# Optimization experiments

Measured on AMD Instinct MI355X. Metric: run time of the kernel, lower is better.

Reference implementation:

```python
import jax, jax.numpy as jnp
import numpy as np
from jax import lax

B, N, FEAT, MID, HID, OUT = 128, 36, 2048, 517, 128, 1024
STEPS, TEMP = 3, 1.0


def setup_inputs() -> dict:
    key = jax.random.key(0)
    ks = jax.random.split(key, 10)
    s = 0.02
    return {
        "boxes": jax.random.uniform(ks[0], (B, 4, N), jnp.float32),
        "attention": jax.random.normal(ks[1], (B, N), jnp.float32),
        "features": jax.random.normal(ks[2], (B, N, FEAT), jnp.float32),
        "conv_w": jax.random.normal(ks[3], (MID - 5, FEAT), jnp.float32) * s,
        "conv_b": jnp.zeros((MID - 5,), jnp.float32),
        "skew_wx": jax.random.normal(ks[4], (HID, MID), jnp.float32) * s,
        "skew_wy": jax.random.normal(ks[5], (HID, MID), jnp.float32) * s,
        "skew_b1": jnp.zeros((HID,), jnp.float32),
        "skew_w2": jax.random.normal(ks[6], (HID,), jnp.float32) * s,
        "skew_b2": jnp.zeros((1,), jnp.float32),
        "w_ih": jax.random.normal(ks[7], (4 * OUT, MID), jnp.float32) * s,
        "w_hh": jax.random.normal(ks[8], (4 * OUT, OUT), jnp.float32) * s,
        "b_ih": jnp.zeros((4 * OUT,), jnp.float32),
        "b_hh": jnp.zeros((4 * OUT,), jnp.float32),
        "lr": jnp.ones((1,), jnp.float32),
    }


def _calculate_assignment(C, lr_abs, temp, steps):
    # C: (b, n, n) skew-symmetric ordering costs.
    logits = jnp.zeros_like(C)
    for _ in range(steps):
        P = jax.nn.softmax(logits / temp, axis=-1)  # position i -> distribution over elements l
        cum = jnp.cumsum(P, axis=1)                 # sum over positions k <= i
        below = cum - P                             # sum_{k<i} P_kl
        above = cum[:, -1:, :] - cum                # sum_{k>i} P_kl
        # grad_{ij} = sum_l C_{jl} * (above - below)_{il}  (uses skew-symmetry of C)
        G = jnp.einsum('bil,bjl->bij', above - below, C)
        logits = logits - lr_abs * G
    return jax.nn.softmax(logits / temp, axis=-1)


def reference(boxes, attention, features, conv_w, conv_b, skew_wx, skew_wy,
              skew_b1, skew_w2, skew_b2, w_ih, w_hh, b_ih, b_hh, lr):
    b = boxes.shape[0]
    # normalize boxes by per-sample max
    boxes = boxes / jnp.max(boxes.reshape(b, -1), axis=1)[:, None, None]
    # pointwise Conv1: 2048 -> MID-5, features arrives as (b, n, 2048)
    f = jnp.einsum('bnf,mf->bmn', features, conv_w) + conv_b[None, :, None]
    att = attention[:, None, :]                      # (b, 1, n)
    feats = jnp.concatenate([boxes, att, f], axis=1)  # (b, MID, n)
    # PairwiseSkew: f(x_i, x_j) - f(x_j, x_i); the first 1x1-conv over concatenated
    # pairs splits into two linear maps so we never materialize (b, 2*MID, n, n).
    hx = jnp.einsum('hm,bmn->bhn', skew_wx, feats)
    hy = jnp.einsum('hm,bmn->bhn', skew_wy, feats)
    h = jax.nn.relu(hx[:, :, :, None] + hy[:, :, None, :] + skew_b1[None, :, None, None])
    out = jnp.einsum('h,bhij->bij', skew_w2, h) + skew_b2[0]  # (b, n, n)
    C = out - jnp.swapaxes(out, 1, 2)  # skew-symmetrize
    A = _calculate_assignment(C, jnp.abs(lr)[0], TEMP, STEPS)
    # gate features by sigmoid(attention) and apply soft permutation
    gated = feats * jax.nn.sigmoid(att)               # (b, MID, n)
    x = jnp.einsum('bcl,bil->bci', gated, A)          # (b, MID, n)
    x_seq = jnp.transpose(x, (2, 0, 1))               # (n, b, MID)
    # single-layer LSTM (PyTorch gate order i, f, g, o); return final cell state
    bias = b_ih + b_hh
    Hd = w_hh.shape[1]
    def step(carry, xt):
        h_, c_ = carry
        gates = xt @ w_ih.T + h_ @ w_hh.T + bias
        i, fg, g, o = jnp.split(gates, 4, axis=-1)
        c_ = jax.nn.sigmoid(fg) * c_ + jax.nn.sigmoid(i) * jnp.tanh(g)
        h_ = jax.nn.sigmoid(o) * jnp.tanh(c_)
        return (h_, c_), None
    init = (jnp.zeros((b, Hd), x.dtype), jnp.zeros((b, Hd), x.dtype))
    (_, c_fin), _ = lax.scan(step, init, x_seq)
    return c_fin
```

## Files before the change

kernel.cpp:

```cpp
#include <hip/hip_runtime.h>
#include <math.h>

#define NB 128
#define NN 36
#define S37 37
#define S40 40
#define NFEAT 2048
#define NMID 517
#define KP 544
#define NHID 128
#define NOUT 1024
#define ROWS (NB*NN)

typedef __bf16 bf16x8 __attribute__((ext_vector_type(8)));
typedef float  f32x4  __attribute__((ext_vector_type(4)));

__device__ __forceinline__ float sigf(float x){ return 1.f/(1.f+expf(-x)); }
__device__ __forceinline__ unsigned short f2bf(float x){
    unsigned u = __float_as_uint(x);
    return (unsigned short)((u + 0x7FFFu + ((u>>16)&1u)) >> 16);
}
__device__ __forceinline__ float bf2f(unsigned short b){
    return __uint_as_float(((unsigned)b) << 16);
}

__global__ __launch_bounds__(256) void prep_all(
    const float* __restrict__ boxes, const float* __restrict__ att,
    const float* __restrict__ features, const float* __restrict__ conv_w,
    const float* __restrict__ wx, const float* __restrict__ wy,
    const float* __restrict__ b1, const float* __restrict__ w_ih,
    const float* __restrict__ w_hh, const float* __restrict__ b_ih,
    const float* __restrict__ b_hh,
    unsigned short* __restrict__ features_bf, unsigned short* __restrict__ convw_bf,
    unsigned short* __restrict__ wxy_bf, float* __restrict__ hxy_b,
    unsigned short* __restrict__ wih_il, unsigned short* __restrict__ whh_il,
    float* __restrict__ comb_b, unsigned short* __restrict__ h0,
    float* __restrict__ c, float* __restrict__ feats)
{
    int gtid = blockIdx.x*256 + threadIdx.x;
    int gs = gridDim.x*256;
    if (gtid < 128*64) {
        int b = gtid >> 6, t = gtid & 63;
        float mx = -1e30f;
        for (int idx = t; idx < 4*NN; idx += 64) mx = fmaxf(mx, boxes[b*4*NN + idx]);
        for (int off = 32; off > 0; off >>= 1) mx = fmaxf(mx, __shfl_down(mx, off));
        mx = __shfl(mx, 0);
        float inv = 1.f / mx;
        for (int idx = t; idx < 4*NN; idx += 64) {
            int r = idx / NN, n = idx - r*NN;
            feats[(size_t)(b*NN+n)*NMID + r] = boxes[b*4*NN + idx] * inv;
        }
        if (t < NN) feats[(size_t)(b*NN+t)*NMID + 4] = att[b*NN + t];
    }
    for (int i = gtid; i < ROWS*NFEAT; i += gs) features_bf[i] = f2bf(features[i]);
    for (int i = gtid; i < 512*NFEAT; i += gs) convw_bf[i] = f2bf(conv_w[i]);
    for (int i = gtid; i < 256*KP; i += gs) {
        int r = i / KP, k = i - r*KP;
        float v = 0.f;
        if (k < NMID) v = (r < NHID) ? wx[(size_t)r*NMID+k] : wy[(size_t)(r-NHID)*NMID+k];
        wxy_bf[i] = f2bf(v);
    }
    for (int i = gtid; i < 256; i += gs) hxy_b[i] = (i < NHID) ? b1[i] : 0.f;
    for (int i = gtid; i < 4*NOUT*KP; i += gs) {
        int row = i / KP, k = i - row*KP;
        int u = row >> 2, g = row & 3;
        wih_il[i] = (k < NMID) ? f2bf(w_ih[(size_t)(g*NOUT+u)*NMID + k]) : (unsigned short)0;
    }
    for (int i = gtid; i < 4*NOUT*NOUT; i += gs) {
        int row = i >> 10, k = i & 1023;
        int u = row >> 2, g = row & 3;
        whh_il[i] = f2bf(w_hh[(size_t)(g*NOUT+u)*NOUT + k]);
    }
    for (int i = gtid; i < 4*NOUT; i += gs) {
        int u = i >> 2, g = i & 3;
        comb_b[i] = b_ih[g*NOUT+u] + b_hh[g*NOUT+u];
    }
    for (int i = gtid; i < NB*NOUT; i += gs) { h0[i] = 0; c[i] = 0.f; }
}

__global__ __launch_bounds__(256) void gemm128(
    const unsigned short* __restrict__ A, const unsigned short* __restrict__ B,
    const float* __restrict__ bias, void* __restrict__ Cp,
    int Ksl, int lda, int ldb, int ldc, int obf, long long pstride)
{
    __shared__ __align__(16) char As[16384];
    __shared__ __align__(16) char Bs[16384];
    int m0 = blockIdx.y * 128, n0 = blockIdx.x * 128;
    int kbeg = blockIdx.z * Ksl;
    int tid = threadIdx.x;
    int lane = tid & 63, wave = tid >> 6;
    int wm = wave >> 1, wn = wave & 1;
    int sw = ((lane>>4)<<8) + (((lane&15) ^ ((lane>>4)<<2))<<4);
    f32x4 acc[4][4];
    #pragma unroll
    for (int i = 0; i < 4; ++i)
        #pragma unroll
        for (int j = 0; j < 4; ++j) acc[i][j] = (f32x4){0.f,0.f,0.f,0.f};

    for (int k0 = 0; k0 < Ksl; k0 += 32) {
        #pragma unroll
        for (int p = 0; p < 2; ++p) {
            int cc = p*256 + tid;
            int r = cc >> 2, q = cc & 3;
            int sa = ((r>>4)<<10) + (q<<8) + ((((r&15) ^ (q<<2)))<<4);
            uint4 va = *(const uint4*)(A + (size_t)(m0+r)*lda + kbeg + k0 + q*8);
            *(uint4*)(As + sa) = va;
            uint4 vb = *(const uint4*)(B + (size_t)(n0+r)*ldb + kbeg + k0 + q*8);
            *(uint4*)(Bs + sa) = vb;
        }
        __syncthreads();
        bf16x8 af[4], bfr[4];
        #pragma unroll
        for (int i = 0; i < 4; ++i) af[i]  = *(bf16x8*)(As + ((wm*4+i)<<10) + sw);
        #pragma unroll
        for (int j = 0; j < 4; ++j) bfr[j] = *(bf16x8*)(Bs + ((wn*4+j)<<10) + sw);
        #pragma unroll
        for (int i = 0; i < 4; ++i)
            #pragma unroll
            for (int j = 0; j < 4; ++j)
                acc[i][j] = __builtin_amdgcn_mfma_f32_16x16x32_bf16(af[i], bfr[j], acc[i][j], 0, 0, 0);
        __syncthreads();
    }
    int colf = lane & 15, rowq = lane >> 4;
    #pragma unroll
    for (int j = 0; j < 4; ++j) {
        int col = n0 + (wn*4+j)*16 + colf;
        float bv = bias ? bias[col] : 0.f;
        #pragma unroll
        for (int i = 0; i < 4; ++i) {
            #pragma unroll
            for (int reg = 0; reg < 4; ++reg) {
                int row = m0 + (wm*4+i)*16 + rowq*4 + reg;
                float v = acc[i][j][reg] + bv;
                if (obf) ((unsigned short*)Cp)[(size_t)row*ldc + col] = f2bf(v);
                else ((float*)Cp + (size_t)blockIdx.z*pstride)[(size_t)row*ldc + col] = v;
            }
        }
    }
}

__global__ __launch_bounds__(256) void conv_reduce(
    const float* __restrict__ part, const float* __restrict__ bias,
    float* __restrict__ feats, unsigned short* __restrict__ feats_bf)
{
    int gtid = blockIdx.x*256 + threadIdx.x;
    int gs = gridDim.x*256;
    const size_t PS = (size_t)ROWS * 512;
    for (int i = gtid; i < ROWS*512; i += gs) {
        int r = i >> 9, cc = i & 511;
        float s = part[i] + part[PS+i] + part[2*PS+i] + part[3*PS+i] + bias[cc];
        feats[(size_t)r*NMID + 5 + cc] = s;
        feats_bf[(size_t)r*KP + 5 + cc] = f2bf(s);
    }
    for (int i = gtid; i < ROWS*5; i += gs) {
        int r = i / 5, cc = i - r*5;
        feats_bf[(size_t)r*KP + cc] = f2bf(feats[(size_t)r*NMID + cc]);
    }
    for (int i = gtid; i < ROWS*27; i += gs) {
        int r = i / 27, cc = i - r*27;
        feats_bf[(size_t)r*KP + 517 + cc] = 0;
    }
}

__global__ __launch_bounds__(256) void gemm_mfma(
    const unsigned short* __restrict__ A, const unsigned short* __restrict__ B,
    const float* __restrict__ bias, void* __restrict__ Cp,
    int K, int lda, int ldb, int ldc, int obf)
{
    __shared__ __align__(16) char As[8192];
    __shared__ __align__(16) char Bs[4096];
    int m0 = blockIdx.y * 128, n0 = blockIdx.x * 64;
    int tid = threadIdx.x;
    int lane = tid & 63, wave = tid >> 6;
    int wm = wave >> 1, wn = wave & 1;
    f32x4 acc[4][2];
    #pragma unroll
    for (int i = 0; i < 4; ++i)
        #pragma unroll
        for (int j = 0; j < 2; ++j) acc[i][j] = (f32x4){0.f,0.f,0.f,0.f};

    for (int k0 = 0; k0 < K; k0 += 32) {
        #pragma unroll
        for (int cc = tid; cc < 512; cc += 256) {
            int r = cc >> 2, q = cc & 3;
            uint4 v = *(const uint4*)(A + (size_t)(m0+r)*lda + k0 + q*8);
            *(uint4*)(As + ((r>>4)<<10) + (q<<8) + ((r&15)<<4)) = v;
        }
        {
            int r = tid >> 2, q = tid & 3;
            uint4 v = *(const uint4*)(B + (size_t)(n0+r)*ldb + k0 + q*8);
            *(uint4*)(Bs + ((r>>4)<<10) + (q<<8) + ((r&15)<<4)) = v;
        }
        __syncthreads();
        bf16x8 af[4], bfr[2];
        #pragma unroll
        for (int i = 0; i < 4; ++i) af[i]  = *(bf16x8*)(As + ((wm*4+i)<<10) + (lane<<4));
        #pragma unroll
        for (int j = 0; j < 2; ++j) bfr[j] = *(bf16x8*)(Bs + ((wn*2+j)<<10) + (lane<<4));
        #pragma unroll
        for (int i = 0; i < 4; ++i)
            #pragma unroll
            for (int j = 0; j < 2; ++j)
                acc[i][j] = __builtin_amdgcn_mfma_f32_16x16x32_bf16(af[i], bfr[j], acc[i][j], 0, 0, 0);
        __syncthreads();
    }
    int colf = lane & 15, rowq = lane >> 4;
    #pragma unroll
    for (int j = 0; j < 2; ++j) {
        int col = n0 + (wn*2+j)*16 + colf;
        float bv = bias ? bias[col] : 0.f;
        #pragma unroll
        for (int i = 0; i < 4; ++i) {
            #pragma unroll
            for (int reg = 0; reg < 4; ++reg) {
                int row = m0 + (wm*4+i)*16 + rowq*4 + reg;
                float v = acc[i][j][reg] + bv;
                if (obf) ((unsigned short*)Cp)[(size_t)row*ldc + col] = f2bf(v);
                else     ((float*)Cp)[(size_t)row*ldc + col] = v;
            }
        }
    }
}

__global__ __launch_bounds__(256) void out_k(
    const float* __restrict__ hxy, const float* __restrict__ w2,
    float* __restrict__ out_g)
{
    __shared__ float s_hx[9*129], s_hy[NN*129], s_w2[NHID];
    int b = blockIdx.x, i0 = blockIdx.y * 9, tid = threadIdx.x;
    for (int i = tid; i < 9*NHID; i += 256) {
        int n = i >> 7, h = i & 127;
        s_hx[n*129+h] = hxy[(size_t)(b*NN+i0+n)*256 + h];
    }
    for (int i = tid; i < NN*NHID; i += 256) {
        int n = i >> 7, h = i & 127;
        s_hy[n*129+h] = hxy[(size_t)(b*NN+n)*256 + 128 + h];
    }
    if (tid < NHID) s_w2[tid] = w2[tid];
    __syncthreads();
    for (int idx = tid; idx < 9*NN; idx += 256) {
        int il = idx / NN, j = idx - il*NN;
        const float* px = &s_hx[il*129];
        const float* py = &s_hy[j*129];
        float s = 0.f;
        #pragma unroll 8
        for (int h = 0; h < NHID; ++h) s += s_w2[h] * fmaxf(px[h] + py[h], 0.f);
        out_g[(size_t)b*NN*NN + (i0+il)*NN + j] = s;
    }
}

__global__ __launch_bounds__(256) void iter_k(
    const float* __restrict__ out_g, const float* __restrict__ att,
    const float* __restrict__ lr, float* __restrict__ A_g)
{
    __shared__ __align__(16) float s_out[NN*S40], s_C[NN*S40], s_logits[NN*S40], s_P[NN*S40];
    __shared__ float s_sg[NN];
    int b = blockIdx.x, tid = threadIdx.x;
    for (int idx = tid; idx < NN*NN; idx += 256) {
        int i = idx / NN, j = idx - i*NN;
        s_out[i*S40+j] = out_g[(size_t)b*NN*NN + idx];
        s_logits[i*S40+j] = 0.f;
    }
    if (tid < NN) s_sg[tid] = sigf(att[b*NN + tid]);
    float lr_abs = fabsf(lr[0]);
    __syncthreads();
    for (int idx = tid; idx < NN*NN; idx += 256) {
        int i = idx / NN, j = idx - i*NN;
        s_C[i*S40+j] = s_out[i*S40+j] - s_out[j*S40+i];
    }
    __syncthreads();
    for (int it = 0; it < 3; ++it) {
        if (tid < NN) {
            int i = tid;
            float mx = -1e30f;
            for (int l = 0; l < NN; ++l) mx = fmaxf(mx, s_logits[i*S40+l]);
            float sum = 0.f;
            for (int l = 0; l < NN; ++l) { float e = expf(s_logits[i*S40+l]-mx); s_P[i*S40+l] = e; sum += e; }
            float inv = 1.f/sum;
            for (int l = 0; l < NN; ++l) s_P[i*S40+l] *= inv;
        }
        __syncthreads();
        if (tid < NN) {
            int l = tid;
            float S = 0.f;
            for (int i = 0; i < NN; ++i) S += s_P[i*S40+l];
            float cum = 0.f;
            for (int i = 0; i < NN; ++i) {
                float p = s_P[i*S40+l];
                cum += p;
                s_P[i*S40+l] = S - 2.f*cum + p;
            }
        }
        __syncthreads();
        for (int idx = tid; idx < NN*NN; idx += 256) {
            int i = idx / NN, j = idx - i*NN;
            const f32x4* Pp = (const f32x4*)&s_P[i*S40];
            const f32x4* Cc = (const f32x4*)&s_C[j*S40];
            float g = 0.f;
            #pragma unroll
            for (int q = 0; q < 9; ++q) {
                f32x4 a = Pp[q], bb = Cc[q];
                g += a[0]*bb[0] + a[1]*bb[1] + a[2]*bb[2] + a[3]*bb[3];
            }
            s_logits[i*S40+j] -= lr_abs * g;
        }
        __syncthreads();
    }
    if (tid < NN) {
        int i = tid;
        float mx = -1e30f;
        for (int l = 0; l < NN; ++l) mx = fmaxf(mx, s_logits[i*S40+l]);
        float sum = 0.f;
        for (int l = 0; l < NN; ++l) { float e = expf(s_logits[i*S40+l]-mx); s_P[i*S40+l] = e; sum += e; }
        float inv = 1.f/sum;
        for (int l = 0; l < NN; ++l)
            A_g[(size_t)b*NN*NN + i*NN + l] = s_P[i*S40+l] * inv * s_sg[l];
    }
}

__global__ __launch_bounds__(256) void xseq_k(
    const float* __restrict__ feats, const float* __restrict__ A_g,
    unsigned short* __restrict__ xseq)
{
    __shared__ float s_P[NN*S37];
    int b = blockIdx.x, half = blockIdx.y, tid = threadIdx.x;
    for (int idx = tid; idx < NN*NN; idx += 256) {
        int i = idx / NN, l = idx - i*NN;
        s_P[i*S37+l] = A_g[(size_t)b*NN*NN + idx];
    }
    __syncthreads();
    const float* fb = feats + (size_t)b*NN*NMID;
    int ncols = (half == 0 && tid < 32) ? 2 : 1;
    #pragma unroll
    for (int rep = 0; rep < 2; ++rep) {
        if (rep >= ncols) break;
        int c = (rep == 0) ? half*256 + tid : 512 + tid;
        float colv[NN];
        #pragma unroll
        for (int l = 0; l < NN; ++l) colv[l] = (c < NMID) ? fb[l*NMID + c] : 0.f;
        #pragma unroll 4
        for (int i = 0; i < NN; ++i) {
            float s = 0.f;
            #pragma unroll
            for (int l = 0; l < NN; ++l) s += s_P[i*S37+l] * colv[l];
            xseq[((size_t)i*NB + b)*KP + c] = f2bf(s);
        }
    }
}

__global__ __launch_bounds__(256, 2) void lstm_step(
    const unsigned short* __restrict__ h_in, const unsigned short* __restrict__ whh,
    const unsigned short* __restrict__ xw_t, float* __restrict__ c,
    unsigned short* __restrict__ h_out, float* __restrict__ cout)
{
    __shared__ __align__(16) char Bls[65536];
    __shared__ __align__(16) float gates[32][36];
    int tid = threadIdx.x, lane = tid & 63, wave = tid >> 6;
    int bt = blockIdx.x >> 7, ct = blockIdx.x & 127;
    int m0 = bt * 32, n0 = ct * 32;
    #pragma unroll
    for (int r = 0; r < 16; ++r) {
        int idx = r*256 + tid;
        int n = idx >> 7, kc = idx & 127;
        uint4 v = *(const uint4*)(whh + (size_t)(n0+n)*NOUT + kc*8);
        *(uint4*)(Bls + kc*512 + (((n&16) | ((n^kc)&15))<<4)) = v;
    }
    __syncthreads();
    int wm = wave >> 1, wn = wave & 1;
    int q = lane >> 4, ml = lane & 15;
    const unsigned short* hrow = h_in + (size_t)(m0 + wm*16 + ml)*NOUT + q*8;
    int nl = wn*16 + ml;
    f32x4 acc = (f32x4){0.f,0.f,0.f,0.f};
    #pragma unroll 8
    for (int it = 0; it < 32; ++it) {
        int kc = it*4 + q;
        bf16x8 a = *(const bf16x8*)(hrow + it*32);
        bf16x8 b = *(const bf16x8*)(Bls + kc*512 + (((nl&16) | ((nl^kc)&15))<<4));
        acc = __builtin_amdgcn_mfma_f32_16x16x32_bf16(a, b, acc, 0, 0, 0);
    }
    #pragma unroll
    for (int reg = 0; reg < 4; ++reg)
        gates[wm*16 + q*4 + reg][wn*16 + ml] = acc[reg];
    __syncthreads();
    {
        int ul = tid & 7, bl = tid >> 3;
        int b = m0 + bl, u = ct*8 + ul;
        float4 gl = *(const float4*)&gates[bl][ul*4];
        uint2 xw2 = *(const uint2*)(xw_t + (size_t)b*4*NOUT + n0 + ul*4);
        float g0 = gl.x + bf2f((unsigned short)(xw2.x & 0xffffu));
        float g1 = gl.y + bf2f((unsigned short)(xw2.x >> 16));
        float g2 = gl.z + bf2f((unsigned short)(xw2.y & 0xffffu));
        float g3 = gl.w + bf2f((unsigned short)(xw2.y >> 16));
        float ig = sigf(g0), fg = sigf(g1), gg = tanhf(g2), og = sigf(g3);
        size_t o = (size_t)b*NOUT + u;
        float cc = fg*c[o] + ig*gg;
        c[o] = cc;
        if (cout) cout[o] = cc;
        else      h_out[o] = f2bf(og*tanhf(cc));
    }
}

extern "C" void kernel_launch(void* const* d_in, const int* in_sizes, int n_in,
                              void* d_out, int out_size, void* d_ws, size_t ws_size,
                              hipStream_t stream) {
    (void)in_sizes; (void)n_in; (void)out_size; (void)ws_size;
    const float* boxes     = (const float*)d_in[0];
    const float* attention = (const float*)d_in[1];
    const float* features  = (const float*)d_in[2];
    const float* conv_w    = (const float*)d_in[3];
    const float* conv_b    = (const float*)d_in[4];
    const float* skew_wx   = (const float*)d_in[5];
    const float* skew_wy   = (const float*)d_in[6];
    const float* skew_b1   = (const float*)d_in[7];
    const float* skew_w2   = (const float*)d_in[8];
    const float* w_ih      = (const float*)d_in[10];
    const float* w_hh      = (const float*)d_in[11];
    const float* b_ih      = (const float*)d_in[12];
    const float* b_hh      = (const float*)d_in[13];
    const float* lr        = (const float*)d_in[14];

    char* ws = (char*)d_ws;
    float*          part     = (float*)(ws);
    unsigned short* xw_bf    = (unsigned short*)(ws);
    unsigned short* features_bf = (unsigned short*)(ws + 37748736);
    unsigned short* convw_bf = (unsigned short*)(ws + 56623104);
    float*          feats    = (float*)(ws + 58720256);
    float*          hxy      = (float*)(ws + 68249600);
    unsigned short* feats_bf = (unsigned short*)(ws + 72968192);
    unsigned short* xseq_bf  = (unsigned short*)(ws + 77981696);
    unsigned short* wih_il   = (unsigned short*)(ws + 82995200);
    unsigned short* whh_il   = (unsigned short*)(ws + 87451648);
    unsigned short* wxy_bf   = (unsigned short*)(ws + 95840256);
    float*          comb_b   = (float*)(ws + 96118784);
    float*          hxy_b    = (float*)(ws + 96135168);
    unsigned short* h0       = (unsigned short*)(ws + 96136192);
    unsigned short* h1       = (unsigned short*)(ws + 96398336);
    float*          out_g    = (float*)(ws + 96660480);
    float*          A_g      = (float*)(ws + 97324032);
    float*          cst      = (float*)(ws + 97987584);

    prep_all<<<2048, 256, 0, stream>>>(boxes, attention, features, conv_w,
                                       skew_wx, skew_wy, skew_b1, w_ih, w_hh,
                                       b_ih, b_hh, features_bf, convw_bf,
                                       wxy_bf, hxy_b, wih_il, whh_il, comb_b,
                                       h0, cst, feats);
    gemm128<<<dim3(4, 36, 4), 256, 0, stream>>>(features_bf, convw_bf, nullptr,
                                                (void*)part, 512, NFEAT, NFEAT, 512, 0,
                                                (long long)ROWS*512);
    conv_reduce<<<2048, 256, 0, stream>>>(part, conv_b, feats, feats_bf);
    gemm_mfma<<<dim3(4, 36), 256, 0, stream>>>(feats_bf, wxy_bf, hxy_b,
                                               (void*)hxy, KP, KP, KP, 256, 0);
    out_k<<<dim3(NB, 4), 256, 0, stream>>>(hxy, skew_w2, out_g);
    iter_k<<<NB, 256, 0, stream>>>(out_g, attention, lr, A_g);
    xseq_k<<<dim3(NB, 2), 256, 0, stream>>>(feats, A_g, xseq_bf);
    gemm128<<<dim3(32, 36, 1), 256, 0, stream>>>(xseq_bf, wih_il, comb_b,
                                                 (void*)xw_bf, KP, KP, KP, 4*NOUT, 1, 0);
    unsigned short* hbuf[2] = {h0, h1};
    for (int t = 0; t < NN; ++t) {
        float* co = (t == NN-1) ? (float*)d_out : nullptr;
        lstm_step<<<512, 256, 0, stream>>>(hbuf[t & 1], whh_il,
                                           xw_bf + (size_t)t*NB*4*NOUT, cst,
                                           hbuf[(t+1) & 1], co);
    }
}
```

Baseline: 709.3 us.

## Replace per-step LSTM launches with a persistent kernel using grid barriers

The 36 separate lstm_step launches become a single persistent kernel. Each block loads its W_hh tile into LDS once, keeps the cell state in registers, and synchronises with the other blocks in its batch tile after each step through an atomic counter barrier. Step 0 skips the recurrent GEMM because h is zero. This removes launch overhead and repeated W_hh reloads, but it depends on all 512 blocks being co-resident (2 per CU at 64KB LDS), which risks deadlock if they are not.

```diff
diff --git a/kernel.cpp b/kernel.cpp
--- a/kernel.cpp
+++ b/kernel.cpp
@@ -34,8 +34,8 @@
     unsigned short* __restrict__ features_bf, unsigned short* __restrict__ convw_bf,
     unsigned short* __restrict__ wxy_bf, float* __restrict__ hxy_b,
     unsigned short* __restrict__ wih_il, unsigned short* __restrict__ whh_il,
-    float* __restrict__ comb_b, unsigned short* __restrict__ h0,
-    float* __restrict__ c, float* __restrict__ feats)
+    float* __restrict__ comb_b, unsigned int* __restrict__ bar,
+    float* __restrict__ feats)
 {
     int gtid = blockIdx.x*256 + threadIdx.x;
     int gs = gridDim.x*256;
@@ -75,7 +75,7 @@
         int u = i >> 2, g = i & 3;
         comb_b[i] = b_ih[g*NOUT+u] + b_hh[g*NOUT+u];
     }
-    for (int i = gtid; i < NB*NOUT; i += gs) { h0[i] = 0; c[i] = 0.f; }
+    for (int i = gtid; i < 128; i += gs) bar[i] = 0u;
 }
 
 __global__ __launch_bounds__(256) void gemm128(
@@ -348,10 +348,10 @@
     }
 }
 
-__global__ __launch_bounds__(256, 2) void lstm_step(
-    const unsigned short* __restrict__ h_in, const unsigned short* __restrict__ whh,
-    const unsigned short* __restrict__ xw_t, float* __restrict__ c,
-    unsigned short* __restrict__ h_out, float* __restrict__ cout)
+__global__ __launch_bounds__(256, 2) void lstm_persist(
+    const unsigned short* __restrict__ whh, const unsigned short* __restrict__ xw,
+    unsigned short* __restrict__ h0, unsigned short* __restrict__ h1,
+    float* __restrict__ dout, unsigned int* __restrict__ bar)
 {
     __shared__ __align__(16) char Bls[65536];
     __shared__ __align__(16) float gates[32][36];
@@ -365,38 +365,58 @@
         uint4 v = *(const uint4*)(whh + (size_t)(n0+n)*NOUT + kc*8);
         *(uint4*)(Bls + kc*512 + (((n&16) | ((n^kc)&15))<<4)) = v;
     }
-    __syncthreads();
     int wm = wave >> 1, wn = wave & 1;
     int q = lane >> 4, ml = lane & 15;
-    const unsigned short* hrow = h_in + (size_t)(m0 + wm*16 + ml)*NOUT + q*8;
     int nl = wn*16 + ml;
-    f32x4 acc = (f32x4){0.f,0.f,0.f,0.f};
-    #pragma unroll 8
-    for (int it = 0; it < 32; ++it) {
-        int kc = it*4 + q;
-        bf16x8 a = *(const bf16x8*)(hrow + it*32);
-        bf16x8 b = *(const bf16x8*)(Bls + kc*512 + (((nl&16) | ((nl^kc)&15))<<4));
-        acc = __builtin_amdgcn_mfma_f32_16x16x32_bf16(a, b, acc, 0, 0, 0);
-    }
-    #pragma unroll
-    for (int reg = 0; reg < 4; ++reg)
-        gates[wm*16 + q*4 + reg][wn*16 + ml] = acc[reg];
+    int ul = tid & 7, bl = tid >> 3;
+    int b = m0 + bl, u = ct*8 + ul;
+    unsigned int* cnt = bar + bt*32;
+    float cc = 0.f;
     __syncthreads();
-    {
-        int ul = tid & 7, bl = tid >> 3;
-        int b = m0 + bl, u = ct*8 + ul;
-        float4 gl = *(const float4*)&gates[bl][ul*4];
-        uint2 xw2 = *(const uint2*)(xw_t + (size_t)b*4*NOUT + n0 + ul*4);
-        float g0 = gl.x + bf2f((unsigned short)(xw2.x & 0xffffu));
-        float g1 = gl.y + bf2f((unsigned short)(xw2.x >> 16));
-        float g2 = gl.z + bf2f((unsigned short)(xw2.y & 0xffffu));
-        float g3 = gl.w + bf2f((unsigned short)(xw2.y >> 16));
+    for (int t = 0; t < NN; ++t) {
+        const unsigned short* hin = (t & 1) ? h1 : h0;
+        unsigned short*       hw  = (t & 1) ? h0 : h1;
+        uint2 xw2 = *(const uint2*)(xw + ((size_t)t*NB + b)*4*NOUT + n0 + ul*4);
+        float g0 = bf2f((unsigned short)(xw2.x & 0xffffu));
+        float g1 = bf2f((unsigned short)(xw2.x >> 16));
+        float g2 = bf2f((unsigned short)(xw2.y & 0xffffu));
+        float g3 = bf2f((unsigned short)(xw2.y >> 16));
+        if (t > 0) {
+            const unsigned short* hrow = hin + (size_t)(m0 + wm*16 + ml)*NOUT + q*8;
+            f32x4 acc = (f32x4){0.f,0.f,0.f,0.f};
+            #pragma unroll 8
+            for (int it = 0; it < 32; ++it) {
+                int kc = it*4 + q;
+                bf16x8 a = *(const bf16x8*)(hrow + it*32);
+                bf16x8 bb = *(const bf16x8*)(Bls + kc*512 + (((nl&16) | ((nl^kc)&15))<<4));
+                acc = __builtin_amdgcn_mfma_f32_16x16x32_bf16(a, bb, acc, 0, 0, 0);
+            }
+            #pragma unroll
+            for (int reg = 0; reg < 4; ++reg)
+                gates[wm*16 + q*4 + reg][wn*16 + ml] = acc[reg];
+            __syncthreads();
+            float4 gl = *(const float4*)&gates[bl][ul*4];
+            g0 += gl.x; g1 += gl.y; g2 += gl.z; g3 += gl.w;
+        }
         float ig = sigf(g0), fg = sigf(g1), gg = tanhf(g2), og = sigf(g3);
-        size_t o = (size_t)b*NOUT + u;
-        float cc = fg*c[o] + ig*gg;
-        c[o] = cc;
-        if (cout) cout[o] = cc;
-        else      h_out[o] = f2bf(og*tanhf(cc));
+        cc = fg*cc + ig*gg;
+        if (t == NN-1) {
+            dout[(size_t)b*NOUT + u] = cc;
+        } else {
+            hw[(size_t)b*NOUT + u] = f2bf(og*tanhf(cc));
+            __syncthreads();
+            if (tid == 0) {
+                __builtin_amdgcn_fence(__ATOMIC_RELEASE, "agent");
+                __hip_atomic_fetch_add(cnt, 1u, __ATOMIC_RELAXED,
+                                       __HIP_MEMORY_SCOPE_AGENT);
+                unsigned target = 128u * (unsigned)(t + 1);
+                while (__hip_atomic_load(cnt, __ATOMIC_RELAXED,
+                                         __HIP_MEMORY_SCOPE_AGENT) < target)
+                    __builtin_amdgcn_s_sleep(1);
+            }
+            __syncthreads();
+            __builtin_amdgcn_fence(__ATOMIC_ACQUIRE, "agent");
+        }
     }
 }
 
@@ -437,13 +457,13 @@
     unsigned short* h1       = (unsigned short*)(ws + 96398336);
     float*          out_g    = (float*)(ws + 96660480);
     float*          A_g      = (float*)(ws + 97324032);
-    float*          cst      = (float*)(ws + 97987584);
+    unsigned int*   bar      = (unsigned int*)(ws + 97987584);
 
     prep_all<<<2048, 256, 0, stream>>>(boxes, attention, features, conv_w,
                                        skew_wx, skew_wy, skew_b1, w_ih, w_hh,
                                        b_ih, b_hh, features_bf, convw_bf,
                                        wxy_bf, hxy_b, wih_il, whh_il, comb_b,
-                                       h0, cst, feats);
+                                       bar, feats);
     gemm128<<<dim3(4, 36, 4), 256, 0, stream>>>(features_bf, convw_bf, nullptr,
                                                 (void*)part, 512, NFEAT, NFEAT, 512, 0,
                                                 (long long)ROWS*512);
@@ -455,11 +475,6 @@
     xseq_k<<<dim3(NB, 2), 256, 0, stream>>>(feats, A_g, xseq_bf);
     gemm128<<<dim3(32, 36, 1), 256, 0, stream>>>(xseq_bf, wih_il, comb_b,
                                                  (void*)xw_bf, KP, KP, KP, 4*NOUT, 1, 0);
-    unsigned short* hbuf[2] = {h0, h1};
-    for (int t = 0; t < NN; ++t) {
-        float* co = (t == NN-1) ? (float*)d_out : nullptr;
-        lstm_step<<<512, 256, 0, stream>>>(hbuf[t & 1], whh_il,
-                                           xw_bf + (size_t)t*NB*4*NOUT, cst,
-                                           hbuf[(t+1) & 1], co);
-    }
-}
+    lstm_persist<<<512, 256, 0, stream>>>(whh_il, xw_bf,
+                                          h0, h1, (float*)d_out, bar);
+}
```

After: 1.604 ms. +126.2%, slower.
